# Kernel tuning notes

Measured on AMD Instinct MI355X. Metric: run time of the kernel, lower is better.

## Reference

```python
import jax, jax.numpy as jnp
import numpy as np
from jax import lax

STRIDE = 16
RATIOS = (0.5, 1.0, 2.0)
SCALES = (128.0, 256.0, 512.0)


def _anchor_template():
    # template[i] = [stride/2, stride/2, w, h], i = ri*3 + si
    r = jnp.asarray(RATIOS, jnp.float32)[:, None]        # (3,1)
    s = jnp.asarray(SCALES, jnp.float32)[None, :]        # (1,3)
    sqrt_r = jnp.sqrt(r)
    w = (s / sqrt_r)                                     # (3,3)
    h = (s * sqrt_r)
    half = jnp.full_like(w, STRIDE / 2.0)
    return jnp.stack([half, half, w, h], axis=-1).reshape(9, 4)  # (9,4) xywh


def setup_inputs() -> dict:
    key = jax.random.key(0)
    ks = jax.random.split(key, 6)
    B, C, H, W = 8, 512, 50, 76
    feature_maps = jax.random.normal(ks[0], (B, C, H, W), jnp.float32)
    conv_w = jax.random.normal(ks[1], (512, 512, 3, 3), jnp.float32) * 0.01
    conv_b = jnp.zeros((512,), jnp.float32)
    cls_w = jax.random.normal(ks[2], (18, 512, 1, 1), jnp.float32) * 0.01
    cls_b = jnp.zeros((18,), jnp.float32)
    reg_w = jax.random.normal(ks[3], (36, 512, 1, 1), jnp.float32) * 0.01
    reg_b = jnp.zeros((36,), jnp.float32)
    # (width, height) per image; x is clamped to im_size[0], y to im_size[1]
    img_size = jnp.tile(jnp.array([[W * STRIDE, H * STRIDE]], jnp.int32), (B, 1))
    return {"feature_maps": feature_maps, "conv_w": conv_w, "conv_b": conv_b,
            "cls_w": cls_w, "cls_b": cls_b, "reg_w": reg_w, "reg_b": reg_b,
            "img_size": img_size}


def reference(feature_maps, conv_w, conv_b, cls_w, cls_b, reg_w, reg_b, img_size):
    B, C, H, W = feature_maps.shape
    # 3x3 conv, pad=1, stride=1 + ReLU
    f = lax.conv_general_dilated(feature_maps, conv_w, (1, 1), 'SAME',
                                 dimension_numbers=('NCHW', 'OIHW', 'NCHW'))
    f = jax.nn.relu(f + conv_b[None, :, None, None])
    # 1x1 heads, then NCHW -> BHWC (matches the two torch transposes)
    cls = jnp.einsum('bchw,oc->bhwo', f, cls_w.reshape(18, 512)) + cls_b
    reg = jnp.einsum('bchw,oc->bhwo', f, reg_w.reshape(36, 512)) + reg_b
    cls = cls.reshape(B, H, W, 9, 2)
    reg = reg.reshape(B, H, W, 9, 4)

    # Vectorized anchor generation (replaces nested hi/wi loops)
    tmpl = _anchor_template()                              # (9,4)
    sx = (jnp.arange(W, dtype=jnp.float32) * STRIDE)[None, :]   # (1,W)
    sy = (jnp.arange(H, dtype=jnp.float32) * STRIDE)[:, None]   # (H,1)
    zeros = jnp.zeros((H, W), jnp.float32)
    shift = jnp.stack([jnp.broadcast_to(sx, (H, W)),
                       jnp.broadcast_to(sy, (H, W)), zeros, zeros], axis=-1)  # (H,W,4)
    anchors = tmpl[None, None] + shift[:, :, None, :]      # (H,W,9,4)
    anchors = jnp.broadcast_to(anchors, (B, H, W, 9, 4)).reshape(B, -1, 4)

    cls = cls.reshape(B, -1, 2)
    reg = reg.reshape(B, -1, 4)

    # anchor2bbox: inverse of the target encoding in loss()
    axy, awh = anchors[..., :2], anchors[..., 2:]
    pxy = axy + reg[..., :2] * awh
    pwh = awh * jnp.exp(reg[..., 2:])

    # eval-mode clip to image bounds (vectorized over batch)
    im = img_size.astype(jnp.float32)[:, None, :]          # (B,1,2) = (w,h)
    x1y1 = pxy - pwh / 2
    x2y2 = x1y1 + pwh
    x1y1 = jnp.clip(x1y1, 0.0, im)
    x2y2 = jnp.clip(x2y2, 0.0, im)
    wh = x2y2 - x1y1
    cxy = x1y1 + wh / 2
    proposals = jnp.concatenate([cxy, wh], axis=-1)        # (B, H*W*9, 4)
    return (proposals, cls)
```

## Files before the change

kernel.cpp:

```cpp
#include <hip/hip_runtime.h>

typedef __attribute__((ext_vector_type(8))) __bf16 bf16x8;
typedef __attribute__((ext_vector_type(4))) float  f32x4;

#define GPTR(p)   (__attribute__((address_space(1))) void*)(p)
#define LDSPTR(p) (__attribute__((address_space(3))) void*)(p)
#define MFMA16 __builtin_amdgcn_mfma_f32_16x16x32_bf16
#define SB() __builtin_amdgcn_sched_barrier(0)

__device__ __forceinline__ unsigned short f2bf(float f) {
    union { float f; unsigned u; } v; v.f = f;
    unsigned r = v.u + 0x7FFF + ((v.u >> 16) & 1);
    return (unsigned short)(r >> 16);
}

#define MTOT   30400
#define MPAD   30464
#define KTOT   4608
#define NT     72

__global__ __launch_bounds__(256) void pad_transpose(
    const float* __restrict__ in, unsigned short* __restrict__ P)
{
    __shared__ float t[32][33];
    const int tx = threadIdx.x;
    const int ty = threadIdx.y;
    const int tix = blockIdx.x % 3;
    const int cix = blockIdx.x / 3;
    const int y = blockIdx.y;
    const int b = blockIdx.z;
    const int x0 = tix * 32, c0 = cix * 32;

    const int x = x0 + tx;
    if (x < 76) {
#pragma unroll
        for (int i = 0; i < 4; ++i) {
            int c = c0 + ty + i * 8;
            t[ty + i * 8][tx] = in[((b * 512 + c) * 50 + y) * 76 + x];
        }
    }
    __syncthreads();
#pragma unroll
    for (int i = 0; i < 4; ++i) {
        int xr = ty + i * 8;
        int xw = x0 + xr;
        if (xw < 76) {
            P[((b * 52 + y + 1) * 78 + (xw + 1)) * 512 + c0 + tx] = f2bf(t[tx][xr]);
        }
    }
}

__global__ __launch_bounds__(256) void border_zero(unsigned short* __restrict__ P)
{
    int i = blockIdx.x * 256 + threadIdx.x;
    int b   = i >> 14;
    int rem = i & 16383;
    int seg = rem >> 6;
    int c8  = (rem & 63) << 3;
    int y, x;
    if (seg < 78)       { y = 0;  x = seg; }
    else if (seg < 156) { y = 51; x = seg - 78; }
    else if (seg < 206) { y = seg - 155; x = 0; }
    else                { y = seg - 205; x = 77; }
    *(float4*)(P + ((b * 52 + y) * 78 + x) * 512 + c8) = make_float4(0.f, 0.f, 0.f, 0.f);
}

__global__ __launch_bounds__(256) void wt_transform(
    const float* __restrict__ cw,
    const float* __restrict__ cls_w, const float* __restrict__ reg_w,
    const float* __restrict__ cls_b, const float* __restrict__ reg_b,
    unsigned short* __restrict__ Wt,
    unsigned short* __restrict__ W2, float* __restrict__ b2)
{
    int bid = blockIdx.x;
    if (bid < 9216) {
        int i = bid * 256 + threadIdx.x;
        int o = i / KTOT;
        int r = i - o * KTOT;
        int kk = r >> 9;
        int c  = r & 511;
        Wt[i] = f2bf(cw[(o * 512 + c) * 9 + kk]);
    } else {
        int i = (bid - 9216) * 256 + threadIdx.x;
        int n = i >> 9, k = i & 511;
        float v = 0.f;
        if (n < 18) v = cls_w[n * 512 + k];
        else if (n < 54) v = reg_w[(n - 18) * 512 + k];
        W2[i] = f2bf(v);
        if (i < 64) {
            float bv = 0.f;
            if (i < 18) bv = cls_b[i];
            else if (i < 54) bv = reg_b[i - 18];
            b2[i] = bv;
        }
    }
}

__global__ __launch_bounds__(512, 2) void conv_gemm8(
    const unsigned short* __restrict__ P,
    const unsigned short* __restrict__ Wt,
    const float* __restrict__ bias,
    unsigned short* __restrict__ F)
{
    __shared__ __attribute__((aligned(1024))) unsigned char lds[131072];

    const int tid = threadIdx.x;
    const int l   = tid & 63;
    const int w   = tid >> 6;
    const int wr  = w >> 2;
    const int nc  = w & 3;
    const int hB  = nc >> 1;
    const int rB  = (nc & 1) * 4;

    const int orig = blockIdx.y * 119 + blockIdx.x;
    const int xcd = orig & 7, seq = orig >> 3;
    const int wg  = (xcd < 6 ? xcd * 30 : 180 + (xcd - 6) * 29) + seq;
    const int m0  = (wg % 119) * 256;
    const int n0  = (wg / 119) * 256;

    const int loff = (l & 15) * 64 + (((l >> 4) * 16) ^ ((l & 8) ? 32 : 0));
    const int kelS = ((l & 3) * 8) ^ ((l & 32) ? 16 : 0);

    int cbA[2][2], nbB[2][2];
#pragma unroll
    for (int h = 0; h < 2; ++h)
#pragma unroll
        for (int j = 0; j < 2; ++j) {
            const int s    = j * 8 + w;
            const int rowt = h * 128 + (s >> 1) * 16 + (l >> 2);
            int m = m0 + rowt; if (m >= MTOT) m = 0;
            int b = m / 3800; int r = m - b * 3800;
            int y = r / 76;   int x = r - y * 76;
            cbA[h][j] = ((b * 52 + y + 1) * 78 + (x + 1)) * 512 + (s & 1) * 32 + kelS;
            nbB[h][j] = (n0 + rowt) * KTOT + (s & 1) * 32 + kelS;
        }

    auto stA = [&](int t, int h, unsigned char* abase) {
        const int kk  = t >> 3;
        const int tap = ((kk / 3 - 1) * 78 + (kk % 3 - 1)) * 512 + (t & 7) * 64;
#pragma unroll
        for (int j = 0; j < 2; ++j)
            __builtin_amdgcn_global_load_lds(GPTR(P + cbA[h][j] + tap),
                LDSPTR(abase + h * 16384 + j * 8192 + w * 1024), 16, 0, 0);
    };
    auto stB = [&](int t, int h, unsigned char* bbase) {
#pragma unroll
        for (int j = 0; j < 2; ++j)
            __builtin_amdgcn_global_load_lds(GPTR(Wt + nbB[h][j] + t * 64),
                LDSPTR(bbase + h * 16384 + j * 8192 + w * 1024), 16, 0, 0);
    };

    f32x4 acc[8][4];
#pragma unroll
    for (int i = 0; i < 8; ++i)
#pragma unroll
        for (int j = 0; j < 4; ++j) acc[i][j] = (f32x4){0.f, 0.f, 0.f, 0.f};

#define RD(basep, subR, ks) (*(const bf16x8*)((basep) + (((subR) * 2 + (ks)) * 1024) + loff))

    {
        unsigned char* A0b = lds;
        unsigned char* B0b = lds + 32768;
        stB(0, 0, B0b); stB(0, 1, B0b); stA(0, 0, A0b); stA(0, 1, A0b);
        __syncthreads();
    }

    for (int g = 0; g < NT; ++g) {
        unsigned char* Ac = lds + (g & 1) * 65536;
        unsigned char* Bc = Ac + 32768;
        unsigned char* An = lds + (((g & 1) ^ 1)) * 65536;
        unsigned char* Bn = An + 32768;
        unsigned char* Ah = Ac + wr * 16384;
        unsigned char* Bh = Bc + hB * 16384;

        if (g + 1 < NT) {
            stB(g + 1, 0, Bn); stB(g + 1, 1, Bn);
            stA(g + 1, 0, An); stA(g + 1, 1, An);
        }
        SB();

#pragma unroll
        for (int ks = 0; ks < 2; ++ks) {
            bf16x8 a[8], b[4];
#pragma unroll
            for (int f = 0; f < 8; ++f) a[f] = RD(Ah, f, ks);
#pragma unroll
            for (int n = 0; n < 4; ++n) b[n] = RD(Bh, rB + n, ks);
#pragma unroll
            for (int n = 0; n < 4; ++n)
#pragma unroll
                for (int f = 0; f < 8; ++f)
                    acc[f][n] = MFMA16(a[f], b[n], acc[f][n], 0, 0, 0);
        }

        __syncthreads();
    }
#undef RD

#pragma unroll
    for (int ni = 0; ni < 4; ++ni) {
        const int col = n0 + nc * 64 + ni * 16 + (l & 15);
        const float bcol = bias[col];
#pragma unroll
        for (int mi = 0; mi < 8; ++mi) {
#pragma unroll
            for (int jj = 0; jj < 4; ++jj) {
                const int row = m0 + wr * 128 + mi * 16 + (l >> 4) * 4 + jj;
                if (row < MTOT)
                    F[row * 512 + col] = f2bf(fmaxf(acc[mi][ni][jj] + bcol, 0.f));
            }
        }
    }
}

__global__ __launch_bounds__(256) void head_decode(
    const unsigned short* __restrict__ F,
    const unsigned short* __restrict__ W2,
    const float* __restrict__ b2,
    const int* __restrict__ img,
    float* __restrict__ out)
{
    __shared__ float S[64][56];
    const int tid  = threadIdx.x;
    const int lane = tid & 63;
    const int wv   = tid >> 6;
    const int mblk = blockIdx.x * 64;
    const int arow = mblk + wv * 16 + (lane & 15);

    f32x4 acc[4];
#pragma unroll
    for (int ni = 0; ni < 4; ++ni) acc[ni] = (f32x4){0.f, 0.f, 0.f, 0.f};

#pragma unroll 4
    for (int ks = 0; ks < 16; ++ks) {
        const int kloc = ks * 32 + (lane >> 4) * 8;
        bf16x8 a = *(const bf16x8*)(F + arow * 512 + kloc);
#pragma unroll
        for (int ni = 0; ni < 4; ++ni) {
            bf16x8 b = *(const bf16x8*)(W2 + (ni * 16 + (lane & 15)) * 512 + kloc);
            acc[ni] = MFMA16(a, b, acc[ni], 0, 0, 0);
        }
    }

#pragma unroll
    for (int ni = 0; ni < 4; ++ni) {
        int col = ni * 16 + (lane & 15);
        if (col < 54) {
            float bb = b2[col];
#pragma unroll
            for (int j = 0; j < 4; ++j)
                S[wv * 16 + (lane >> 4) * 4 + j][col] = acc[ni][j] + bb;
        }
    }
    __syncthreads();

    for (int it = tid; it < 576; it += 256) {
        int rowl = it / 9;
        int a    = it - rowl * 9;
        int m = mblk + rowl;
        if (m >= MTOT) continue;
        int b   = m / 3800;
        int rem = m - b * 3800;
        int y = rem / 76;
        int x = rem - y * 76;

        int ri = a / 3, si = a - ri * 3;
        float sqr = (ri == 0) ? 0.70710678118654752f : ((ri == 1) ? 1.f : 1.41421356237309515f);
        float scale = (float)(128 << si);
        float wa = scale / sqr;
        float ha = scale * sqr;
        float ax = (float)x * 16.f + 8.f;
        float ay = (float)y * 16.f + 8.f;

        float r0 = S[rowl][18 + a * 4 + 0];
        float r1 = S[rowl][18 + a * 4 + 1];
        float r2 = S[rowl][18 + a * 4 + 2];
        float r3 = S[rowl][18 + a * 4 + 3];

        float px = ax + r0 * wa;
        float py = ay + r1 * ha;
        float pw = wa * expf(r2);
        float ph = ha * expf(r3);

        float x1 = px - 0.5f * pw, y1 = py - 0.5f * ph;
        float x2 = x1 + pw,        y2 = y1 + ph;
        float imx = (float)img[2 * b], imy = (float)img[2 * b + 1];
        x1 = fminf(fmaxf(x1, 0.f), imx); x2 = fminf(fmaxf(x2, 0.f), imx);
        y1 = fminf(fmaxf(y1, 0.f), imy); y2 = fminf(fmaxf(y2, 0.f), imy);
        float ww = x2 - x1, hh = y2 - y1;
        float cx = x1 + 0.5f * ww, cy = y1 + 0.5f * hh;

        int pidx = b * 34200 + rem * 9 + a;
        ((float4*)out)[pidx] = make_float4(cx, cy, ww, hh);
        float* oc = out + 1094400 + pidx * 2;
        oc[0] = S[rowl][a * 2 + 0];
        oc[1] = S[rowl][a * 2 + 1];
    }
}

extern "C" void kernel_launch(void* const* d_in, const int* in_sizes, int n_in,
                              void* d_out, int out_size, void* d_ws, size_t ws_size,
                              hipStream_t stream) {
    const float* fm     = (const float*)d_in[0];
    const float* conv_w = (const float*)d_in[1];
    const float* conv_b = (const float*)d_in[2];
    const float* cls_w  = (const float*)d_in[3];
    const float* cls_b  = (const float*)d_in[4];
    const float* reg_w  = (const float*)d_in[5];
    const float* reg_b  = (const float*)d_in[6];
    const int*   img    = (const int*)d_in[7];
    float* out = (float*)d_out;

    char* ws = (char*)d_ws;
    unsigned short* P  = (unsigned short*)(ws);
    unsigned short* Wt = (unsigned short*)(ws + 33226752);
    unsigned short* F  = (unsigned short*)(ws + 37945344);
    unsigned short* W2 = (unsigned short*)(ws + 69140480);
    float*          b2 = (float*)(ws + 69206016);

    hipMemsetAsync((char*)F + (size_t)MTOT * 512 * 2, 0, (size_t)(MPAD - MTOT) * 512 * 2, stream);

    border_zero<<<512, 256, 0, stream>>>(P);
    pad_transpose<<<dim3(48, 50, 8), dim3(32, 8, 1), 0, stream>>>(fm, P);
    wt_transform<<<9344, 256, 0, stream>>>(conv_w, cls_w, reg_w, cls_b, reg_b, Wt, W2, b2);
    conv_gemm8<<<dim3(119, 2), 512, 0, stream>>>(P, Wt, conv_b, F);
    head_decode<<<476, 256, 0, stream>>>(F, W2, b2, img, out);
}
```

Measured before the change: 198.2 us.

## Shrink conv GEMM tile to 128x128 with 4 waves and finer K steps

Replaces the 256x256-tile, 8-wave conv GEMM with a 128x128-tile, 4-wave kernel that steps K by 32 instead of 64 and uses 32 KB of LDS instead of 128 KB. It launches 952 workgroups instead of 238, so more blocks fit on each CU and the 256 CUs are filled more evenly. The intent is better occupancy and latency hiding. In exchange, each block reuses loaded data less, global and L2 traffic rises, and there are twice as many barrier iterations per block. The XCD remap is simplified to a plain modulo-8 interleave.

```diff
diff --git a/kernel.cpp b/kernel.cpp
--- a/kernel.cpp
+++ b/kernel.cpp
@@ -17,7 +17,7 @@
 #define MTOT   30400
 #define MPAD   30464
 #define KTOT   4608
-#define NT     72
+#define NT2    144
 
 __global__ __launch_bounds__(256) void pad_transpose(
     const float* __restrict__ in, unsigned short* __restrict__ P)
@@ -96,102 +96,86 @@
     }
 }
 
-__global__ __launch_bounds__(512, 2) void conv_gemm8(
+__global__ __launch_bounds__(256, 4) void conv_gemm4(
     const unsigned short* __restrict__ P,
     const unsigned short* __restrict__ Wt,
     const float* __restrict__ bias,
     unsigned short* __restrict__ F)
 {
-    __shared__ __attribute__((aligned(1024))) unsigned char lds[131072];
+    __shared__ __attribute__((aligned(1024))) unsigned char lds[32768];
 
     const int tid = threadIdx.x;
     const int l   = tid & 63;
     const int w   = tid >> 6;
-    const int wr  = w >> 2;
-    const int nc  = w & 3;
-    const int hB  = nc >> 1;
-    const int rB  = (nc & 1) * 4;
-
-    const int orig = blockIdx.y * 119 + blockIdx.x;
-    const int xcd = orig & 7, seq = orig >> 3;
-    const int wg  = (xcd < 6 ? xcd * 30 : 180 + (xcd - 6) * 29) + seq;
-    const int m0  = (wg % 119) * 256;
-    const int n0  = (wg / 119) * 256;
+    const int wr  = w >> 1;
+    const int nc  = w & 1;
+
+    const int orig = blockIdx.y * 238 + blockIdx.x;
+    const int wg   = (orig & 7) * 119 + (orig >> 3);
+    const int m0   = (wg % 238) * 128;
+    const int n0   = (wg / 238) * 128;
 
     const int loff = (l & 15) * 64 + (((l >> 4) * 16) ^ ((l & 8) ? 32 : 0));
     const int kelS = ((l & 3) * 8) ^ ((l & 32) ? 16 : 0);
 
-    int cbA[2][2], nbB[2][2];
-#pragma unroll
-    for (int h = 0; h < 2; ++h)
-#pragma unroll
-        for (int j = 0; j < 2; ++j) {
-            const int s    = j * 8 + w;
-            const int rowt = h * 128 + (s >> 1) * 16 + (l >> 2);
-            int m = m0 + rowt; if (m >= MTOT) m = 0;
-            int b = m / 3800; int r = m - b * 3800;
-            int y = r / 76;   int x = r - y * 76;
-            cbA[h][j] = ((b * 52 + y + 1) * 78 + (x + 1)) * 512 + (s & 1) * 32 + kelS;
-            nbB[h][j] = (n0 + rowt) * KTOT + (s & 1) * 32 + kelS;
-        }
-
-    auto stA = [&](int t, int h, unsigned char* abase) {
-        const int kk  = t >> 3;
-        const int tap = ((kk / 3 - 1) * 78 + (kk % 3 - 1)) * 512 + (t & 7) * 64;
+    int cbA[2], nbB[2];
+#pragma unroll
+    for (int j = 0; j < 2; ++j) {
+        const int s    = j * 4 + w;
+        const int rowt = s * 16 + (l >> 2);
+        int m = m0 + rowt; if (m >= MTOT) m = 0;
+        int b = m / 3800; int r = m - b * 3800;
+        int y = r / 76;   int x = r - y * 76;
+        cbA[j] = ((b * 52 + y + 1) * 78 + (x + 1)) * 512 + kelS;
+        nbB[j] = (n0 + rowt) * KTOT + kelS;
+    }
+
+    auto stA = [&](int t, unsigned char* abase) {
+        const int kk  = t >> 4;
+        const int tap = ((kk / 3 - 1) * 78 + (kk % 3 - 1)) * 512 + (t & 15) * 32;
 #pragma unroll
         for (int j = 0; j < 2; ++j)
-            __builtin_amdgcn_global_load_lds(GPTR(P + cbA[h][j] + tap),
-                LDSPTR(abase + h * 16384 + j * 8192 + w * 1024), 16, 0, 0);
+            __builtin_amdgcn_global_load_lds(GPTR(P + cbA[j] + tap),
+                LDSPTR(abase + j * 4096 + w * 1024), 16, 0, 0);
     };
-    auto stB = [&](int t, int h, unsigned char* bbase) {
+    auto stB = [&](int t, unsigned char* bbase) {
+        const int koff = t * 32;
 #pragma unroll
         for (int j = 0; j < 2; ++j)
-            __builtin_amdgcn_global_load_lds(GPTR(Wt + nbB[h][j] + t * 64),
-                LDSPTR(bbase + h * 16384 + j * 8192 + w * 1024), 16, 0, 0);
+            __builtin_amdgcn_global_load_lds(GPTR(Wt + nbB[j] + koff),
+                LDSPTR(bbase + j * 4096 + w * 1024), 16, 0, 0);
     };
 
-    f32x4 acc[8][4];
-#pragma unroll
-    for (int i = 0; i < 8; ++i)
+    f32x4 acc[4][4];
+#pragma unroll
+    for (int i = 0; i < 4; ++i)
 #pragma unroll
         for (int j = 0; j < 4; ++j) acc[i][j] = (f32x4){0.f, 0.f, 0.f, 0.f};
 
-#define RD(basep, subR, ks) (*(const bf16x8*)((basep) + (((subR) * 2 + (ks)) * 1024) + loff))
-
-    {
-        unsigned char* A0b = lds;
-        unsigned char* B0b = lds + 32768;
-        stB(0, 0, B0b); stB(0, 1, B0b); stA(0, 0, A0b); stA(0, 1, A0b);
-        __syncthreads();
-    }
-
-    for (int g = 0; g < NT; ++g) {
-        unsigned char* Ac = lds + (g & 1) * 65536;
-        unsigned char* Bc = Ac + 32768;
-        unsigned char* An = lds + (((g & 1) ^ 1)) * 65536;
-        unsigned char* Bn = An + 32768;
-        unsigned char* Ah = Ac + wr * 16384;
-        unsigned char* Bh = Bc + hB * 16384;
-
-        if (g + 1 < NT) {
-            stB(g + 1, 0, Bn); stB(g + 1, 1, Bn);
-            stA(g + 1, 0, An); stA(g + 1, 1, An);
-        }
+#define RD(basep, subR) (*(const bf16x8*)((basep) + ((subR) * 1024) + loff))
+
+    stB(0, lds + 8192); stA(0, lds);
+    __syncthreads();
+
+    for (int g = 0; g < NT2; ++g) {
+        unsigned char* Ac = lds + (g & 1) * 16384;
+        unsigned char* Bc = Ac + 8192;
+        unsigned char* An = lds + (((g & 1) ^ 1)) * 16384;
+        unsigned char* Bn = An + 8192;
+
+        if (g + 1 < NT2) { stB(g + 1, Bn); stA(g + 1, An); }
         SB();
 
-#pragma unroll
-        for (int ks = 0; ks < 2; ++ks) {
-            bf16x8 a[8], b[4];
-#pragma unroll
-            for (int f = 0; f < 8; ++f) a[f] = RD(Ah, f, ks);
-#pragma unroll
-            for (int n = 0; n < 4; ++n) b[n] = RD(Bh, rB + n, ks);
-#pragma unroll
-            for (int n = 0; n < 4; ++n)
-#pragma unroll
-                for (int f = 0; f < 8; ++f)
-                    acc[f][n] = MFMA16(a[f], b[n], acc[f][n], 0, 0, 0);
-        }
+        bf16x8 a[4], b[4];
+#pragma unroll
+        for (int f = 0; f < 4; ++f) a[f] = RD(Ac, wr * 4 + f);
+#pragma unroll
+        for (int n = 0; n < 4; ++n) b[n] = RD(Bc, nc * 4 + n);
+#pragma unroll
+        for (int n = 0; n < 4; ++n)
+#pragma unroll
+            for (int f = 0; f < 4; ++f)
+                acc[f][n] = MFMA16(a[f], b[n], acc[f][n], 0, 0, 0);
 
         __syncthreads();
     }
@@ -202,10 +186,10 @@
         const int col = n0 + nc * 64 + ni * 16 + (l & 15);
         const float bcol = bias[col];
 #pragma unroll
-        for (int mi = 0; mi < 8; ++mi) {
+        for (int mi = 0; mi < 4; ++mi) {
 #pragma unroll
             for (int jj = 0; jj < 4; ++jj) {
-                const int row = m0 + wr * 128 + mi * 16 + (l >> 4) * 4 + jj;
+                const int row = m0 + wr * 64 + mi * 16 + (l >> 4) * 4 + jj;
                 if (row < MTOT)
                     F[row * 512 + col] = f2bf(fmaxf(acc[mi][ni][jj] + bcol, 0.f));
             }
@@ -323,6 +307,6 @@
     border_zero<<<512, 256, 0, stream>>>(P);
     pad_transpose<<<dim3(48, 50, 8), dim3(32, 8, 1), 0, stream>>>(fm, P);
     wt_transform<<<9344, 256, 0, stream>>>(conv_w, cls_w, reg_w, cls_b, reg_b, Wt, W2, b2);
-    conv_gemm8<<<dim3(119, 2), 512, 0, stream>>>(P, Wt, conv_b, F);
+    conv_gemm4<<<dim3(238, 4), 256, 0, stream>>>(P, Wt, conv_b, F);
     head_decode<<<476, 256, 0, stream>>>(F, W2, b2, img, out);
 }
```

Result: slower. 257.1 us (+29.7%).
